# Optimization experiments

Hardware: AMD Instinct MI355X
Metric: run time of the kernel (lower is better)

The kernel has to match this reference:

```python
import jax, jax.numpy as jnp
import numpy as np

C = 256
CQK = C // 8
EPS_NORM = 1e-12  # torch F.normalize eps
EPS_TEMP = 1e-6


def _xavier(key, shape):
    fan_out, fan_in = shape
    limit = float(np.sqrt(6.0 / (fan_in + fan_out)))
    return jax.random.uniform(key, shape, jnp.float32, -limit, limit)


def setup_inputs() -> dict:
    key = jax.random.key(0)
    ks = jax.random.split(key, 6)
    x = jax.random.normal(ks[0], (8, C, 64, 64), jnp.float32)
    Wq = _xavier(ks[1], (CQK, C))
    Wk = _xavier(ks[2], (CQK, C))
    # value conv uses default Conv2d init (kaiming uniform); any random init is fine for a numeric baseline
    bound = float(1.0 / np.sqrt(C))
    Wv = jax.random.uniform(ks[3], (C, C), jnp.float32, -bound, bound)
    bq = jax.random.uniform(ks[4], (CQK,), jnp.float32, -bound, bound)
    bk = jax.random.uniform(ks[5], (CQK,), jnp.float32, -bound, bound)
    bv = jax.random.uniform(jax.random.fold_in(key, 7), (C,), jnp.float32, -bound, bound)
    gamma = jnp.ones((1,), jnp.float32)
    temperature = jnp.array(1.0, jnp.float32)
    return {"x": x, "Wq": Wq, "bq": bq, "Wk": Wk, "bk": bk, "Wv": Wv, "bv": bv,
            "gamma": gamma, "temperature": temperature}


def _l2norm_lastdim(t):
    # F.normalize(p=2, dim=-1): divide by max(||t||_2, eps) along last axis
    n = jnp.sqrt(jnp.sum(t * t, axis=-1, keepdims=True))
    return t / jnp.maximum(n, EPS_NORM)


def reference(x, Wq, bq, Wk, bk, Wv, bv, gamma, temperature):
    B, Cc, H, W = x.shape
    N = H * W
    xf = x.reshape(B, Cc, N)  # (B, C, N)
    # 1x1 convs == channel GEMMs
    q = jnp.einsum('oc,bcn->bon', Wq, xf) + bq[:, None]   # (B, C/8, N)
    k = jnp.einsum('oc,bcn->bon', Wk, xf) + bk[:, None]   # (B, C/8, N)
    v = jnp.einsum('oc,bcn->bon', Wv, xf) + bv[:, None]   # (B, C, N)
    # NOTE: normalization is over the SPATIAL dim (dim=-1), matching the source
    qn = _l2norm_lastdim(q)
    kn = _l2norm_lastdim(k)
    energy = jnp.einsum('bcn,bcm->bnm', qn, kn) / (temperature + EPS_TEMP)
    energy = energy + jnp.eye(N, dtype=energy.dtype)
    attention = jax.nn.softmax(energy, axis=-1)  # (B, N, N)
    # out[b,c,m] = sum_n v[b,c,n] * attention[b,m,n]
    out = jnp.einsum('bcn,bmn->bcm', v, attention)
    out = out.reshape(B, Cc, H, W)
    return gamma * out + x
```

## Files before the change

### kernel.cpp

```cpp
#include <hip/hip_runtime.h>
#include <hip/hip_bf16.h>
#include <math.h>

typedef __attribute__((ext_vector_type(8))) short short8;
typedef __attribute__((ext_vector_type(4))) float floatx4;
typedef __attribute__((ext_vector_type(16))) float floatx16;

#define B_ 8
#define C_ 256
#define N_ 4096
#define LOG2E 1.4426950408889634f
#define XSTRIDE 548

static __device__ __forceinline__ unsigned short f2bf(float f) {
  union { float f; unsigned int u; } v; v.f = f;
  unsigned int u = v.u;
  u += 0x7FFFu + ((u >> 16) & 1u);
  return (unsigned short)(u >> 16);
}
static __device__ __forceinline__ float bf2f(unsigned short h) {
  union { unsigned int u; float f; } v; v.u = ((unsigned int)h) << 16; return v.f;
}
static __device__ __forceinline__ unsigned int pk2(float a, float b) {
  return __builtin_amdgcn_perm(__float_as_uint(b), __float_as_uint(a), 0x07060302u);
}

__global__ void prep_kernel(const float* __restrict__ Wq, const float* __restrict__ Wk,
                            const float* __restrict__ Wv,
                            unsigned short* __restrict__ wqb, unsigned short* __restrict__ wkb,
                            unsigned short* __restrict__ wvb, float* __restrict__ ssq) {
  int t = blockIdx.x * 256 + threadIdx.x;
  if (t < 512) ssq[t] = 0.0f;
  if (t < 8192) { wqb[t] = f2bf(Wq[t]); wkb[t] = f2bf(Wk[t]); }
  int tv = t - 8192;
  if (tv >= 0 && tv < 65536) wvb[tv] = f2bf(Wv[tv]);
}

__launch_bounds__(512, 4)
__global__ void qkv_kernel(const float* __restrict__ x,
                           const unsigned short* __restrict__ wqb,
                           const unsigned short* __restrict__ wkb,
                           const unsigned short* __restrict__ wvb,
                           const float* __restrict__ bq, const float* __restrict__ bk,
                           const float* __restrict__ bv,
                           unsigned short* __restrict__ qbf, unsigned short* __restrict__ kbf,
                           unsigned char* __restrict__ vbf, float* __restrict__ ssq) {
  __shared__ __align__(16) char Xt[64 * XSTRIDE];
  int b = blockIdx.x & 7;
  int nblk = blockIdx.x >> 3;
  int tid = threadIdx.x;
  int w = tid >> 6, lane = tid & 63;
  int r = lane & 15, g = lane >> 4;
  int nh = w & 3, ch = w >> 2;
  int n0 = nblk * 64;

  {
    int q = tid & 15, cpw = tid >> 4;
    const float* xb = x + ((size_t)b << 20) + n0 + q * 4;
    #pragma unroll
    for (int p = 0; p < 4; ++p) {
      int cp = p * 32 + cpw;
      const float* s0 = xb + ((size_t)(2 * cp) << 12);
      float4 a  = *(const float4*)s0;
      float4 bb = *(const float4*)(s0 + 4096);
      char* dst = Xt + cp * 4;
      *(unsigned int*)(dst + (q * 4 + 0) * XSTRIDE) = pk2(a.x, bb.x);
      *(unsigned int*)(dst + (q * 4 + 1) * XSTRIDE) = pk2(a.y, bb.y);
      *(unsigned int*)(dst + (q * 4 + 2) * XSTRIDE) = pk2(a.z, bb.z);
      *(unsigned int*)(dst + (q * 4 + 3) * XSTRIDE) = pk2(a.w, bb.w);
    }
  }
  __syncthreads();

  short8 xf[8];
  #pragma unroll
  for (int ks = 0; ks < 8; ++ks) {
    const char* src = Xt + (nh * 16 + r) * XSTRIDE + (ks * 32 + g * 8) * 2;
    union { unsigned int u[4]; short8 s8; } t;
    t.u[0] = *(const unsigned int*)(src);
    t.u[1] = *(const unsigned int*)(src + 4);
    t.u[2] = *(const unsigned int*)(src + 8);
    t.u[3] = *(const unsigned int*)(src + 12);
    xf[ks] = t.s8;
  }
  int nw = n0 + nh * 16;
  floatx4 zero = {0.f, 0.f, 0.f, 0.f};
  unsigned char* vt = vbf + (size_t)b * C_ * N_;
  const unsigned short* wqk = ch ? wkb : wqb;
  const float* bias = ch ? bk : bq;
  unsigned short* qkdst = ch ? kbf : qbf;
  int sbase = ch ? 256 : 0;

  const unsigned short* vwb = wvb + (size_t)(ch * 128 + r) * 256 + g * 8;
  const unsigned short* qwb = wqk + (size_t)r * 256 + g * 8;

  short8 wf[2][4];
  #pragma unroll
  for (int j = 0; j < 4; ++j) wf[0][j] = *(const short8*)(vwb + j * 32);

  int n = nw + r;
  size_t vsb = (size_t)(n >> 5) * 8192 + ((n >> 3) & 1) * 16 + ((n >> 4) & 1) * 8 + (n & 7);

  #pragma unroll
  for (int t = 0; t < 10; ++t) {
    const unsigned short* curb = (t < 8) ? (vwb + t * 4096) : (qwb + (t - 8) * 4096);
    const unsigned short* nxtb = (t < 7) ? (vwb + (t + 1) * 4096)
                                         : ((t < 9) ? (qwb + (t - 7) * 4096) : curb);
    floatx4 acc = zero;
    #pragma unroll
    for (int j = 0; j < 4; ++j) wf[1][j] = *(const short8*)(curb + (4 + j) * 32);
    #pragma unroll
    for (int j = 0; j < 4; ++j)
      acc = __builtin_amdgcn_mfma_f32_16x16x32_bf16(wf[0][j], xf[j], acc, 0, 0, 0);
    #pragma unroll
    for (int j = 0; j < 4; ++j) wf[0][j] = *(const short8*)(nxtb + j * 32);
    #pragma unroll
    for (int j = 0; j < 4; ++j)
      acc = __builtin_amdgcn_mfma_f32_16x16x32_bf16(wf[1][j], xf[4 + j], acc, 0, 0, 0);

    if (t < 8) {
      int otile = ch * 8 + t;
      #pragma unroll
      for (int rr = 0; rr < 4; ++rr) {
        int oc = otile * 16 + g * 4 + rr;
        float val = acc[rr] + bv[oc];
        int pk8 = __builtin_amdgcn_cvt_pk_fp8_f32(val, val, 0, false);
        vt[vsb + (size_t)oc * 32] = (unsigned char)(pk8 & 0xFF);
      }
    } else {
      #pragma unroll
      for (int rr = 0; rr < 4; ++rr) {
        int oc = (t - 8) * 16 + g * 4 + rr;
        float val = acc[rr] + bias[oc];
        qkdst[(size_t)(b * N_ + nw + r) * 32 + oc] = f2bf(val);
        float s = val * val;
        s += __shfl_xor(s, 1);
        s += __shfl_xor(s, 2);
        s += __shfl_xor(s, 4);
        s += __shfl_xor(s, 8);
        if (r == 0) atomicAdd(&ssq[sbase + b * 32 + oc], s);
      }
    }
  }
}

__launch_bounds__(256, 2)
__global__ void attn_kernel(const unsigned short* __restrict__ qbf,
                            const unsigned short* __restrict__ kbf,
                            const unsigned char* __restrict__ vbf,
                            const float* __restrict__ ssq, const float* __restrict__ temp,
                            const float* __restrict__ x, const float* __restrict__ gamma,
                            float* __restrict__ out) {
  int b = blockIdx.x & 7, mblk = blockIdx.x >> 3;
  int tid = threadIdx.x;
  int w = tid >> 6, lane = tid & 63, c = lane & 31, h = lane >> 5;
  int ms = w & 1, cvh = w >> 1;
  const unsigned short* qb = qbf + (size_t)b * N_ * 32;
  const unsigned short* kb = kbf + (size_t)b * N_ * 32;
  const unsigned char* vt = vbf + (size_t)b * C_ * N_;
  int mrow = mblk * 64 + ms * 32 + c;
  int tdiag = mblk * 2 + ms;

  float invt = LOG2E / (temp[0] + 1e-6f);
  short8 q0r = *(const short8*)&qb[mrow * 32 + h * 8];
  short8 q1r = *(const short8*)&qb[mrow * 32 + 16 + h * 8];
  short8 qf0, qf1;
  #pragma unroll
  for (int j = 0; j < 8; ++j) {
    int ch0 = h * 8 + j, ch1 = 16 + h * 8 + j;
    float s0 = invt * rsqrtf(fmaxf(ssq[b * 32 + ch0] * ssq[256 + b * 32 + ch0], 1e-24f));
    float s1 = invt * rsqrtf(fmaxf(ssq[b * 32 + ch1] * ssq[256 + b * 32 + ch1], 1e-24f));
    ((unsigned short*)&qf0)[j] = f2bf(bf2f(((const unsigned short*)&q0r)[j]) * s0);
    ((unsigned short*)&qf1)[j] = f2bf(bf2f(((const unsigned short*)&q1r)[j]) * s1);
  }

  const unsigned short* kp = kb + (size_t)c * 32 + h * 8;
  const unsigned char* vp = vt + (size_t)(cvh * 128 + c) * 32 + h * 16;

  floatx16 minit;
  #pragma unroll
  for (int i = 0; i < 16; ++i) minit[i] = -2.0f * LOG2E;
  floatx16 zero16 = {0,0,0,0,0,0,0,0,0,0,0,0,0,0,0,0};
  floatx16 acc[4] = {zero16, zero16, zero16, zero16};
  float Lp = 0.0f;
  short8 kfA[2], kfB[2], afA[4], afB[4];

  kfA[0] = *(const short8*)kp;
  kfA[1] = *(const short8*)(kp + 16);
  kp += 1024;
  #pragma unroll
  for (int cvt = 0; cvt < 4; ++cvt)
    afA[cvt] = *(const short8*)(vp + cvt * 1024);
  vp += 8192;

  auto body = [&](int t, short8 (&kfC)[2], short8 (&kfN)[2],
                  short8 (&afC)[4], short8 (&afN)[4]) {
    if (t + 1 < 128) {
      kfN[0] = *(const short8*)kp;
      kfN[1] = *(const short8*)(kp + 16);
      kp += 1024;
      #pragma unroll
      for (int cvt = 0; cvt < 4; ++cvt)
        afN[cvt] = *(const short8*)(vp + cvt * 1024);
      vp += 8192;
    }
    floatx16 s = __builtin_amdgcn_mfma_f32_32x32x16_bf16(kfC[0], qf0, minit, 0, 0, 0);
    s = __builtin_amdgcn_mfma_f32_32x32x16_bf16(kfC[1], qf1, s, 0, 0, 0);
    if (t == tdiag && ((c >> 2) & 1) == h)
      s[(c & 3) | ((c >> 3) << 2)] += LOG2E;
    float p[16];
    #pragma unroll
    for (int i = 0; i < 16; ++i) p[i] = __builtin_amdgcn_exp2f(s[i]);
    Lp += (((p[0] + p[1]) + (p[2] + p[3])) + ((p[4] + p[5]) + (p[6] + p[7])))
        + (((p[8] + p[9]) + (p[10] + p[11])) + ((p[12] + p[13]) + (p[14] + p[15])));
    #pragma unroll
    for (int t16 = 0; t16 < 2; ++t16) {
      int d0 = __builtin_amdgcn_cvt_pk_fp8_f32(p[8*t16+0], p[8*t16+1], 0, false);
      d0 = __builtin_amdgcn_cvt_pk_fp8_f32(p[8*t16+2], p[8*t16+3], d0, true);
      int d1 = __builtin_amdgcn_cvt_pk_fp8_f32(p[8*t16+4], p[8*t16+5], 0, false);
      d1 = __builtin_amdgcn_cvt_pk_fp8_f32(p[8*t16+6], p[8*t16+7], d1, true);
      asm volatile("v_permlane32_swap_b32 %0, %1" : "+v"(d1), "+v"(d0));
      long bl = (long)(((unsigned long long)(unsigned)d1 << 32) | (unsigned)d0);
      #pragma unroll
      for (int cvt = 0; cvt < 4; ++cvt) {
        union { short8 s8; long l[2]; } u; u.s8 = afC[cvt];
        acc[cvt] = __builtin_amdgcn_mfma_f32_32x32x16_fp8_fp8(u.l[t16], bl, acc[cvt], 0, 0, 0);
      }
    }
  };

  #pragma unroll 1
  for (int t = 0; t < 128; t += 2) {
    body(t, kfA, kfB, afA, afB);
    body(t + 1, kfB, kfA, afB, afA);
  }

  Lp += __shfl_xor(Lp, 32);
  float linv = 1.0f / Lp;
  float gam = gamma[0];
  #pragma unroll
  for (int cvt = 0; cvt < 4; ++cvt)
    #pragma unroll
    for (int i = 0; i < 16; ++i) {
      int cv = cvh * 128 + cvt * 32 + (i & 3) + 8 * (i >> 2) + 4 * h;
      size_t idx = ((size_t)(b * C_ + cv) << 12) + mrow;
      out[idx] = gam * acc[cvt][i] * linv + x[idx];
    }
}

extern "C" void kernel_launch(void* const* d_in, const int* in_sizes, int n_in,
                              void* d_out, int out_size, void* d_ws, size_t ws_size,
                              hipStream_t stream) {
  (void)in_sizes; (void)n_in; (void)out_size; (void)ws_size;
  const float* x    = (const float*)d_in[0];
  const float* Wq   = (const float*)d_in[1];
  const float* bq   = (const float*)d_in[2];
  const float* Wk   = (const float*)d_in[3];
  const float* bk   = (const float*)d_in[4];
  const float* Wv   = (const float*)d_in[5];
  const float* bv   = (const float*)d_in[6];
  const float* gam  = (const float*)d_in[7];
  const float* temp = (const float*)d_in[8];
  float* out = (float*)d_out;

  char* ws = (char*)d_ws;
  unsigned char* vbf  = (unsigned char*)ws;
  unsigned short* qbf = (unsigned short*)(ws + (16u << 20));
  unsigned short* kbf = (unsigned short*)(ws + (18u << 20));
  unsigned short* wqb = (unsigned short*)(ws + (20u << 20));
  unsigned short* wkb = wqb + 8192;
  unsigned short* wvb = wkb + 8192;
  float* ssq = (float*)(wvb + 65536);

  prep_kernel<<<dim3(288), dim3(256), 0, stream>>>(Wq, Wk, Wv, wqb, wkb, wvb, ssq);
  qkv_kernel<<<dim3(512), dim3(512), 0, stream>>>(x, wqb, wkb, wvb, bq, bk, bv, qbf, kbf, vbf, ssq);
  attn_kernel<<<dim3(512), dim3(256), 0, stream>>>(qbf, kbf, vbf, ssq, temp, x, gam, out);
}
```

Measured before the change: 158.7 us.

## Deepen K/V prefetch to two tiles ahead and compute row sums via MFMA

Replaces the double-buffered K/V fragment prefetch with a four-slot ring that issues loads two tiles ahead, giving global loads more time to arrive before use. The per-lane scalar accumulation of softmax denominators (16 adds per tile plus a cross-lane shuffle) is replaced by an extra fp8 MFMA that multiplies the probability fragment by a vector of ones. The row sum is then read directly from the accumulator. This trades VALU work for one extra matrix op per half-tile, uses more registers for the prefetch buffers, and sums the fp8-quantized probabilities so the normalizer is computed from the same values used in the output accumulation.

```diff
diff --git a/kernel.cpp b/kernel.cpp
--- a/kernel.cpp
+++ b/kernel.cpp
@@ -182,20 +182,14 @@
   for (int i = 0; i < 16; ++i) minit[i] = -2.0f * LOG2E;
   floatx16 zero16 = {0,0,0,0,0,0,0,0,0,0,0,0,0,0,0,0};
   floatx16 acc[4] = {zero16, zero16, zero16, zero16};
-  float Lp = 0.0f;
-  short8 kfA[2], kfB[2], afA[4], afB[4];
-
-  kfA[0] = *(const short8*)kp;
-  kfA[1] = *(const short8*)(kp + 16);
-  kp += 1024;
-  #pragma unroll
-  for (int cvt = 0; cvt < 4; ++cvt)
-    afA[cvt] = *(const short8*)(vp + cvt * 1024);
-  vp += 8192;
-
-  auto body = [&](int t, short8 (&kfC)[2], short8 (&kfN)[2],
-                  short8 (&afC)[4], short8 (&afN)[4]) {
-    if (t + 1 < 128) {
+  floatx16 accL = zero16;
+  const long ones8 = 0x3838383838383838L;
+
+  short8 kf[4][2];
+  short8 af[4][4];
+
+  auto issue = [&](int t, short8 (&kfN)[2], short8 (&afN)[4]) {
+    if (t < 128) {
       kfN[0] = *(const short8*)kp;
       kfN[1] = *(const short8*)(kp + 16);
       kp += 1024;
@@ -204,6 +198,8 @@
         afN[cvt] = *(const short8*)(vp + cvt * 1024);
       vp += 8192;
     }
+  };
+  auto compute = [&](int t, short8 (&kfC)[2], short8 (&afC)[4]) {
     floatx16 s = __builtin_amdgcn_mfma_f32_32x32x16_bf16(kfC[0], qf0, minit, 0, 0, 0);
     s = __builtin_amdgcn_mfma_f32_32x32x16_bf16(kfC[1], qf1, s, 0, 0, 0);
     if (t == tdiag && ((c >> 2) & 1) == h)
@@ -211,8 +207,6 @@
     float p[16];
     #pragma unroll
     for (int i = 0; i < 16; ++i) p[i] = __builtin_amdgcn_exp2f(s[i]);
-    Lp += (((p[0] + p[1]) + (p[2] + p[3])) + ((p[4] + p[5]) + (p[6] + p[7])))
-        + (((p[8] + p[9]) + (p[10] + p[11])) + ((p[12] + p[13]) + (p[14] + p[15])));
     #pragma unroll
     for (int t16 = 0; t16 < 2; ++t16) {
       int d0 = __builtin_amdgcn_cvt_pk_fp8_f32(p[8*t16+0], p[8*t16+1], 0, false);
@@ -221,6 +215,7 @@
       d1 = __builtin_amdgcn_cvt_pk_fp8_f32(p[8*t16+6], p[8*t16+7], d1, true);
       asm volatile("v_permlane32_swap_b32 %0, %1" : "+v"(d1), "+v"(d0));
       long bl = (long)(((unsigned long long)(unsigned)d1 << 32) | (unsigned)d0);
+      accL = __builtin_amdgcn_mfma_f32_32x32x16_fp8_fp8(ones8, bl, accL, 0, 0, 0);
       #pragma unroll
       for (int cvt = 0; cvt < 4; ++cvt) {
         union { short8 s8; long l[2]; } u; u.s8 = afC[cvt];
@@ -229,14 +224,18 @@
     }
   };
 
+  issue(0, kf[0], af[0]);
+  issue(1, kf[1], af[1]);
+
   #pragma unroll 1
-  for (int t = 0; t < 128; t += 2) {
-    body(t, kfA, kfB, afA, afB);
-    body(t + 1, kfB, kfA, afB, afA);
-  }
-
-  Lp += __shfl_xor(Lp, 32);
-  float linv = 1.0f / Lp;
+  for (int t = 0; t < 128; t += 4) {
+    issue(t + 2, kf[2], af[2]);  compute(t + 0, kf[0], af[0]);
+    issue(t + 3, kf[3], af[3]);  compute(t + 1, kf[1], af[1]);
+    issue(t + 4, kf[0], af[0]);  compute(t + 2, kf[2], af[2]);
+    issue(t + 5, kf[1], af[1]);  compute(t + 3, kf[3], af[3]);
+  }
+
+  float linv = 1.0f / accL[0];
   float gam = gamma[0];
   #pragma unroll
   for (int cvt = 0; cvt < 4; ++cvt)
```

Measured after the change: 158.7 us. About the same (-0.0%).
